# Performance work log

Measured on AMD Instinct MI355X. Metric: run time of the kernel, lower is better.

## Reference

```python
import jax, jax.numpy as jnp
import numpy as np

N_NODES, N_EDGES = 50000, 800000
IN_DIM, HID, HEADS, OUT_DIM = 256, 32, 8, 16
NEG_SLOPE = 0.2  # PyG GATConv default leaky-relu slope
EPS = 1e-16      # PyG softmax denominator epsilon


def setup_inputs() -> dict:
    key = jax.random.key(0)
    ks = jax.random.split(key, 12)
    x = jax.random.normal(ks[0], (N_NODES, IN_DIM), dtype=jnp.float32)
    edge_index = jax.random.randint(ks[1], (2, N_EDGES), 0, N_NODES, dtype=jnp.int32)
    s1 = 1.0 / np.sqrt(IN_DIM)
    s2 = 1.0 / np.sqrt(HID * HEADS)
    return {
        "x": x,
        "edge_index": edge_index,
        "W1": jax.random.normal(ks[2], (IN_DIM, HEADS * HID), dtype=jnp.float32) * s1,
        "att_src1": jax.random.normal(ks[3], (HEADS, HID), dtype=jnp.float32) * s1,
        "att_dst1": jax.random.normal(ks[4], (HEADS, HID), dtype=jnp.float32) * s1,
        "bias1": jnp.zeros((HEADS * HID,), dtype=jnp.float32),
        "W2": jax.random.normal(ks[5], (HEADS * HID, HEADS * OUT_DIM), dtype=jnp.float32) * s2,
        "att_src2": jax.random.normal(ks[6], (HEADS, OUT_DIM), dtype=jnp.float32) * s2,
        "att_dst2": jax.random.normal(ks[7], (HEADS, OUT_DIM), dtype=jnp.float32) * s2,
        "bias2": jnp.zeros((OUT_DIM,), dtype=jnp.float32),
    }


def _gat_conv(x, src, dst, W, att_src, att_dst, bias, concat):
    # x: [N, F_in]; src/dst: [E'] (self-loops already appended)
    N = x.shape[0]
    H, C = att_src.shape
    h = (x @ W).reshape(N, H, C)                      # [N, H, C]
    a_src = jnp.einsum('nhc,hc->nh', h, att_src)      # [N, H]
    a_dst = jnp.einsum('nhc,hc->nh', h, att_dst)
    e = a_src[src] + a_dst[dst]                       # [E', H]
    e = jax.nn.leaky_relu(e, NEG_SLOPE)
    # segment softmax over edges grouped by destination node
    m = jax.ops.segment_max(e, dst, num_segments=N)   # [N, H]
    e = jnp.exp(e - m[dst])
    denom = jax.ops.segment_sum(e, dst, num_segments=N)
    alpha = e / (denom[dst] + EPS)                    # [E', H]
    msg = h[src] * alpha[:, :, None]                  # [E', H, C] gather+weight
    out = jax.ops.segment_sum(msg, dst, num_segments=N)  # [N, H, C] scatter-add
    if concat:
        out = out.reshape(N, H * C)
    else:
        out = out.mean(axis=1)
    return out + bias


def reference(x, edge_index, W1, att_src1, att_dst1, bias1, W2, att_src2, att_dst2, bias2):
    N = x.shape[0]
    loop = jnp.arange(N, dtype=edge_index.dtype)
    src = jnp.concatenate([edge_index[0], loop])  # PyG add_self_loops=True
    dst = jnp.concatenate([edge_index[1], loop])
    h = _gat_conv(x, src, dst, W1, att_src1, att_dst1, bias1, concat=True)
    h = jax.nn.elu(h)
    out = _gat_conv(h, src, dst, W2, att_src2, att_dst2, bias2, concat=False)
    return out
```

## Files before the change

### kernel.cpp

```cpp
#include <hip/hip_runtime.h>

#define N_NODES 50000
#define N_EDGES 800000
#define EP (N_EDGES + N_NODES)
#define HEADS 8
#define NEG 0.2f

typedef __attribute__((ext_vector_type(8))) short bf16x8;
typedef __attribute__((ext_vector_type(8))) unsigned short u16x8;
typedef __attribute__((ext_vector_type(4))) float f32x4;

#define E_BLOCKS ((EP + 255) / 256)
#define MT_BLOCKS ((N_NODES + 63) / 64)
#define SCAN_BLOCKS 196
#define W_ITEMS  (65536 + 32768)
#define W_BLOCKS ((W_ITEMS + 255) / 256)


__device__ __forceinline__ float bf2f(unsigned short u) {
    return __uint_as_float(((unsigned)u) << 16);
}
__device__ __forceinline__ unsigned short f2bf(float f) {
    unsigned u = __float_as_uint(f);
    return (unsigned short)((u + 0x7FFFu + ((u >> 16) & 1u)) >> 16);
}

__device__ __forceinline__ void get_edge(const int* __restrict__ ei, int e, int& s, int& d) {
    if (e < N_EDGES) { s = ei[e]; d = ei[N_EDGES + e]; }
    else             { s = d = e - N_EDGES; }
}

__device__ __forceinline__ float lrelu(float v) { return v > 0.f ? v : NEG * v; }


__global__ void zero_wprep(int* __restrict__ cnt,
                           const float* __restrict__ W1, const float* __restrict__ W2,
                           unsigned short* __restrict__ W1T, unsigned short* __restrict__ W2T) {
    const int b = blockIdx.x;
    if (b < SCAN_BLOCKS) {
        int idx = b * 256 + threadIdx.x;
        if (idx < N_NODES) cnt[idx] = 0;
    } else {
        int t = (b - SCAN_BLOCKS) * 256 + threadIdx.x;
        if (t < 65536) {
            int k = t >> 8, n = t & 255;
            W1T[n * 256 + k] = f2bf(W1[k * 256 + n]);
        } else if (t < W_ITEMS) {
            int u = t - 65536; int k = u >> 7, n = u & 127;
            W2T[n * 256 + k] = f2bf(W2[k * 128 + n]);
        }
    }
}


__global__ void hist_kernel(const int* __restrict__ ei, int* __restrict__ cnt) {
    int e = blockIdx.x * 256 + threadIdx.x;
    if (e >= EP) return;
    int s, d; get_edge(ei, e, s, d);
    atomicAdd(&cnt[d], 1);
}


__global__ __launch_bounds__(256) void scan_p1(const int* __restrict__ cnt,
                                               int* __restrict__ incl, int* __restrict__ bsum) {
    __shared__ int wsum[4];
    const int tid = threadIdx.x, lane = tid & 63, wid = tid >> 6;
    const int idx = blockIdx.x * 256 + tid;
    int v = (idx < N_NODES) ? cnt[idx] : 0;
#pragma unroll
    for (int off = 1; off < 64; off <<= 1) {
        int t = __shfl_up(v, off);
        if (lane >= off) v += t;
    }
    if (lane == 63) wsum[wid] = v;
    __syncthreads();
    int add = 0;
#pragma unroll
    for (int w = 0; w < 4; w++) add += (w < wid) ? wsum[w] : 0;
    incl[idx] = v + add;
    if (tid == 255) bsum[blockIdx.x] = v + add;
}

__global__ __launch_bounds__(256) void scan_p23(const int* __restrict__ incl,
                                                const int* __restrict__ bsum,
                                                int* __restrict__ cnt_cursor,
                                                int* __restrict__ row_start) {
    __shared__ int sb[256];
    __shared__ int wsum[4];
    const int tid = threadIdx.x, lane = tid & 63, wid = tid >> 6;
    int v = (tid < SCAN_BLOCKS) ? bsum[tid] : 0;
#pragma unroll
    for (int off = 1; off < 64; off <<= 1) {
        int t = __shfl_up(v, off);
        if (lane >= off) v += t;
    }
    if (lane == 63) wsum[wid] = v;
    __syncthreads();
    int add = 0;
#pragma unroll
    for (int w = 0; w < 4; w++) add += (w < wid) ? wsum[w] : 0;
    sb[tid] = v + add;
    __syncthreads();
    const int bex = (blockIdx.x == 0) ? 0 : sb[blockIdx.x - 1];
    const int idx = blockIdx.x * 256 + tid;
    if (idx == 0) row_start[N_NODES] = EP;
    if (idx >= N_NODES) return;
    int ex = bex + incl[idx] - cnt_cursor[idx];
    row_start[idx] = ex;
    cnt_cursor[idx] = ex;
}


template<int NC, int C, bool AF32>
__device__ __forceinline__ void gemm_body(int bx, const void* __restrict__ Aptr,
        const unsigned short* __restrict__ WT,
        const float* __restrict__ att_s, const float* __restrict__ att_d,
        unsigned short* __restrict__ outh,
        float* __restrict__ a_src, float* __restrict__ a_dst) {
    constexpr int WN  = NC / 4;
    constexpr int NT  = WN / 16;
    constexpr int TPH = C / 16;
    constexpr int BJ  = NC / 32;
    __shared__ unsigned short As[64 * 64];
    __shared__ unsigned short Bs[NC * 64];
    const int m0 = bx * 64;
    const int tid  = threadIdx.x;
    const int wave = tid >> 6, lane = tid & 63;
    const int col = lane & 15, quad = lane >> 4;
    const int ar = tid >> 2;
    const int ac = tid & 3;
    const int arow = min(m0 + ar, N_NODES - 1);

    f32x4 acc[4][NT] = {};

    for (int k0 = 0; k0 < 256; k0 += 64) {
        u16x8 av[2];
        if constexpr (AF32) {
            const float* Af = (const float*)Aptr;
#pragma unroll
            for (int j = 0; j < 2; j++) {
                const float* p = Af + (size_t)arow * 256 + k0 + (ac + j * 4) * 8;
                float4 f0 = *(const float4*)p;
                float4 f1 = *(const float4*)(p + 4);
                u16x8 v;
                v[0] = f2bf(f0.x); v[1] = f2bf(f0.y); v[2] = f2bf(f0.z); v[3] = f2bf(f0.w);
                v[4] = f2bf(f1.x); v[5] = f2bf(f1.y); v[6] = f2bf(f1.z); v[7] = f2bf(f1.w);
                av[j] = v;
            }
        } else {
            const unsigned short* Ab = (const unsigned short*)Aptr;
#pragma unroll
            for (int j = 0; j < 2; j++)
                av[j] = *(const u16x8*)(Ab + (size_t)arow * 256 + k0 + (ac + j * 4) * 8);
        }
        u16x8 bv[BJ];
#pragma unroll
        for (int j = 0; j < BJ; j++) {
            int idx = j * 256 + tid, row = idx >> 3, ch = idx & 7;
            bv[j] = *(const u16x8*)(WT + (size_t)row * 256 + k0 + ch * 8);
        }
        __syncthreads();
#pragma unroll
        for (int j = 0; j < 2; j++) {
            int ch = ac + j * 4;
            *(u16x8*)&As[ar * 64 + (ch ^ (ar & 7)) * 8] = av[j];
        }
#pragma unroll
        for (int j = 0; j < BJ; j++) {
            int idx = j * 256 + tid, row = idx >> 3, ch = idx & 7;
            *(u16x8*)&Bs[row * 64 + (ch ^ (row & 7)) * 8] = bv[j];
        }
        __syncthreads();
#pragma unroll
        for (int ks = 0; ks < 64; ks += 32) {
            bf16x8 af[4], bfm[NT];
#pragma unroll
            for (int mi = 0; mi < 4; mi++) {
                int r = mi * 16 + col, c = (ks >> 3) + quad;
                af[mi] = *(const bf16x8*)&As[r * 64 + (c ^ (r & 7)) * 8];
            }
#pragma unroll
            for (int ni = 0; ni < NT; ni++) {
                int r = wave * WN + ni * 16 + col, c = (ks >> 3) + quad;
                bfm[ni] = *(const bf16x8*)&Bs[r * 64 + (c ^ (r & 7)) * 8];
            }
#pragma unroll
            for (int mi = 0; mi < 4; mi++)
#pragma unroll
                for (int ni = 0; ni < NT; ni++)
                    acc[mi][ni] = __builtin_amdgcn_mfma_f32_16x16x32_bf16(
                        af[mi], bfm[ni], acc[mi][ni], 0, 0, 0);
        }
    }

#pragma unroll
    for (int mi = 0; mi < 4; mi++)
#pragma unroll
        for (int ni = 0; ni < NT; ni++)
#pragma unroll
            for (int r = 0; r < 4; r++) {
                int m = m0 + mi * 16 + quad * 4 + r;
                if (m < N_NODES)
                    outh[(size_t)m * NC + wave * WN + ni * 16 + col] = f2bf(acc[mi][ni][r]);
            }

    float asv[NT], adv[NT];
#pragma unroll
    for (int ni = 0; ni < NT; ni++) {
        int n = wave * WN + ni * 16 + col;
        asv[ni] = att_s[n];
        adv[ni] = att_d[n];
    }
#pragma unroll
    for (int mi = 0; mi < 4; mi++)
#pragma unroll
        for (int r = 0; r < 4; r++) {
#pragma unroll
            for (int hl = 0; hl < 2; hl++) {
                float s = 0.f, d = 0.f;
#pragma unroll
                for (int t = 0; t < TPH; t++) {
                    int ni = hl * TPH + t;
                    s = fmaf(acc[mi][ni][r], asv[ni], s);
                    d = fmaf(acc[mi][ni][r], adv[ni], d);
                }
#pragma unroll
                for (int off = 1; off < 16; off <<= 1) {
                    s += __shfl_xor(s, off);
                    d += __shfl_xor(d, off);
                }
                if (col == 0) {
                    int m = m0 + mi * 16 + quad * 4 + r;
                    if (m < N_NODES) {
                        int hh = wave * 2 + hl;
                        a_src[m * 8 + hh] = s;
                        a_dst[m * 8 + hh] = d;
                    }
                }
            }
        }
}


__global__ __launch_bounds__(256) void gemm1_fill(const float* __restrict__ x,
        const unsigned short* __restrict__ W1T,
        const float* __restrict__ att_s, const float* __restrict__ att_d,
        unsigned short* __restrict__ outh,
        float* __restrict__ a_src, float* __restrict__ a_dst,
        const int* __restrict__ ei, int* __restrict__ cursor,
        unsigned short* __restrict__ csr) {
    if (blockIdx.x < MT_BLOCKS) {
        gemm_body<256, 32, true>(blockIdx.x, x, W1T, att_s, att_d, outh, a_src, a_dst);
    } else {
        int e = (blockIdx.x - MT_BLOCKS) * 256 + threadIdx.x;
        if (e >= EP) return;
        int s, d; get_edge(ei, e, s, d);
        int pos = atomicAdd(&cursor[d], 1);
        csr[pos] = (unsigned short)s;
    }
}

__global__ __launch_bounds__(256) void gemm2_kernel(const unsigned short* __restrict__ x2b,
        const unsigned short* __restrict__ W2T,
        const float* __restrict__ att_s, const float* __restrict__ att_d,
        unsigned short* __restrict__ outh,
        float* __restrict__ a_src, float* __restrict__ a_dst) {
    gemm_body<128, 16, false>(blockIdx.x, x2b, W2T, att_s, att_d, outh, a_src, a_dst);
}


__global__ __launch_bounds__(256) void gat_agg_l1(const int* __restrict__ row_start,
        const unsigned short* __restrict__ csr,
        const unsigned short* __restrict__ hfeat, const float* __restrict__ a_src,
        const float* __restrict__ a_dst, const float* __restrict__ bias,
        unsigned short* __restrict__ outp) {
    const int n    = blockIdx.x * 4 + (threadIdx.x >> 6);
    const int lane = threadIdx.x & 63;
    if (n >= N_NODES) return;

    const int rs  = row_start[n];
    const int deg = row_start[n + 1] - rs;
    const int p   = lane >> 5;
    const int q   = lane & 31;
    const int hq  = q >> 2;
    const float adstf = a_dst[n * 8 + hq];

    float acc[8] = {};
    float den = 0.f;

    for (int c0 = 0; c0 < deg; c0 += 64) {
        const int cnt = min(64, deg - c0);
        int myid = (lane < cnt) ? (int)csr[rs + c0 + lane] : 0;
        int e = 0;
        for (; e + 8 <= cnt; e += 8) {
            int ss[4];
#pragma unroll
            for (int j = 0; j < 4; j++) ss[j] = __shfl(myid, e + j * 2 + p);
            float as[4];
#pragma unroll
            for (int j = 0; j < 4; j++) as[j] = a_src[ss[j] * 8 + hq];
            u16x8 v[4];
#pragma unroll
            for (int j = 0; j < 4; j++)
                v[j] = *(const u16x8*)(hfeat + (size_t)ss[j] * 256 + q * 8);
#pragma unroll
            for (int j = 0; j < 4; j++) {
                float w = __expf(lrelu(as[j] + adstf));
                den += w;
#pragma unroll
                for (int k = 0; k < 8; k++)
                    acc[k] = fmaf(w, bf2f(v[j][k]), acc[k]);
            }
        }
        for (; e < cnt; e += 2) {
            int idx = e + p;
            bool ok = idx < cnt;
            int s = __shfl(myid, ok ? idx : cnt - 1);
            float w = ok ? __expf(lrelu(a_src[s * 8 + hq] + adstf)) : 0.f;
            den += w;
            u16x8 v = *(const u16x8*)(hfeat + (size_t)s * 256 + q * 8);
#pragma unroll
            for (int k = 0; k < 8; k++)
                acc[k] = fmaf(w, bf2f(v[k]), acc[k]);
        }
    }

    den += __shfl_xor(den, 32);
#pragma unroll
    for (int k = 0; k < 8; k++) acc[k] += __shfl_xor(acc[k], 32);

    if (p == 0) {
        const float inv = 1.f / (den + 1e-16f);
        float4 b0 = *(const float4*)(bias + q * 8);
        float4 b1 = *(const float4*)(bias + q * 8 + 4);
        float bb[8] = {b0.x, b0.y, b0.z, b0.w, b1.x, b1.y, b1.z, b1.w};
        u16x8 o;
#pragma unroll
        for (int k = 0; k < 8; k++) {
            float v = acc[k] * inv + bb[k];
            o[k] = f2bf(v > 0.f ? v : __expf(v) - 1.f);
        }
        *(u16x8*)(outp + (size_t)n * 256 + q * 8) = o;
    }
}


__global__ __launch_bounds__(256) void gat_agg_l2(const int* __restrict__ row_start,
        const unsigned short* __restrict__ csr,
        const unsigned short* __restrict__ hfeat, const float* __restrict__ a_src,
        const float* __restrict__ a_dst, const float* __restrict__ bias,
        float* __restrict__ outp) {
    const int n    = blockIdx.x * 4 + (threadIdx.x >> 6);
    const int lane = threadIdx.x & 63;
    if (n >= N_NODES) return;

    const int rs  = row_start[n];
    const int deg = row_start[n + 1] - rs;
    const int hf  = lane >> 3;
    const float adstf = a_dst[n * 8 + hf];

    float acc0 = 0.f, acc1 = 0.f, den = 0.f;

    for (int c0 = 0; c0 < deg; c0 += 64) {
        const int cnt = min(64, deg - c0);
        int myid = (lane < cnt) ? (int)csr[rs + c0 + lane] : 0;
        int e = 0;
        for (; e + 8 <= cnt; e += 8) {
            int ss[8];
#pragma unroll
            for (int j = 0; j < 8; j++) ss[j] = __shfl(myid, e + j);
            float as[8];
#pragma unroll
            for (int j = 0; j < 8; j++) as[j] = a_src[ss[j] * 8 + hf];
            ushort2 v[8];
#pragma unroll
            for (int j = 0; j < 8; j++)
                v[j] = *(const ushort2*)(hfeat + (size_t)ss[j] * 128 + lane * 2);
#pragma unroll
            for (int j = 0; j < 8; j++) {
                float w = __expf(lrelu(as[j] + adstf));
                den += w;
                acc0 = fmaf(w, bf2f(v[j].x), acc0);
                acc1 = fmaf(w, bf2f(v[j].y), acc1);
            }
        }
        for (; e < cnt; e++) {
            int s = __shfl(myid, e);
            float w = __expf(lrelu(a_src[s * 8 + hf] + adstf));
            den += w;
            ushort2 hv = *(const ushort2*)(hfeat + (size_t)s * 128 + lane * 2);
            acc0 = fmaf(w, bf2f(hv.x), acc0);
            acc1 = fmaf(w, bf2f(hv.y), acc1);
        }
    }

    const float inv = 1.f / (den + 1e-16f);
    float a0 = acc0 * inv, a1 = acc1 * inv;
#pragma unroll
    for (int off = 8; off <= 32; off <<= 1) {
        a0 += __shfl_xor(a0, off);
        a1 += __shfl_xor(a1, off);
    }
    if (lane < 8) {
        float2 o;
        o.x = a0 * 0.125f + bias[lane * 2 + 0];
        o.y = a1 * 0.125f + bias[lane * 2 + 1];
        *(float2*)(outp + (size_t)n * 16 + lane * 2) = o;
    }
}


extern "C" void kernel_launch(void* const* d_in, const int* in_sizes, int n_in,
                              void* d_out, int out_size, void* d_ws, size_t ws_size,
                              hipStream_t stream) {
    const float* x        = (const float*)d_in[0];
    const int*   ei       = (const int*)d_in[1];
    const float* W1       = (const float*)d_in[2];
    const float* att_src1 = (const float*)d_in[3];
    const float* att_dst1 = (const float*)d_in[4];
    const float* bias1    = (const float*)d_in[5];
    const float* W2       = (const float*)d_in[6];
    const float* att_src2 = (const float*)d_in[7];
    const float* att_dst2 = (const float*)d_in[8];
    const float* bias2    = (const float*)d_in[9];
    float* out = (float*)d_out;

    char* ws = (char*)d_ws;
    unsigned short* h1  = (unsigned short*)(ws);
    unsigned short* h2  = (unsigned short*)(ws);
    unsigned short* x2b = (unsigned short*)(ws + 32ull * 1024 * 1024);
    unsigned short* W1T = (unsigned short*)(ws + 64ull * 1024 * 1024);
    unsigned short* W2T = W1T + 65536;
    char* aux = ws + 66ull * 1024 * 1024;
    float*          a_src     = (float*)(aux);
    float*          a_dst     = (float*)(aux + 1600000);
    int*            row_start = (int*)  (aux + 3200000);
    int*            cnt       = (int*)  (aux + 3400064);
    unsigned short* csr       = (unsigned short*)(aux + 3600128);
    int*            incl      = (int*)  (aux + 5300128);
    int*            bsum      = (int*)  (aux + 5500832);

    const int AGG_BLOCKS = (N_NODES + 3) / 4;

    zero_wprep<<<SCAN_BLOCKS + W_BLOCKS, 256, 0, stream>>>(cnt, W1, W2, W1T, W2T);
    hist_kernel<<<E_BLOCKS, 256, 0, stream>>>(ei, cnt);
    scan_p1<<<SCAN_BLOCKS, 256, 0, stream>>>(cnt, incl, bsum);
    scan_p23<<<SCAN_BLOCKS, 256, 0, stream>>>(incl, bsum, cnt, row_start);

    gemm1_fill<<<MT_BLOCKS + E_BLOCKS, 256, 0, stream>>>(x, W1T, att_src1, att_dst1,
                                                         h1, a_src, a_dst, ei, cnt, csr);
    gat_agg_l1<<<AGG_BLOCKS, 256, 0, stream>>>(row_start, csr, h1, a_src, a_dst, bias1, x2b);

    gemm2_kernel<<<MT_BLOCKS, 256, 0, stream>>>(x2b, W2T, att_src2, att_dst2, h2, a_src, a_dst);
    gat_agg_l2<<<AGG_BLOCKS, 256, 0, stream>>>(row_start, csr, h2, a_src, a_dst, bias2, out);
}
```

Measured before the change: 333.5 us.

## Pre-convert x to bf16 and load GEMM fragments directly from global memory

```diff
diff --git a/kernel.cpp b/kernel.cpp
--- a/kernel.cpp
+++ b/kernel.cpp
@@ -13,6 +13,7 @@
 #define E_BLOCKS ((EP + 255) / 256)
 #define MT_BLOCKS ((N_NODES + 63) / 64)
 #define SCAN_BLOCKS 196
+#define X_BLOCKS 12500
 #define W_ITEMS  (65536 + 32768)
 #define W_BLOCKS ((W_ITEMS + 255) / 256)
 
@@ -33,15 +34,22 @@
 __device__ __forceinline__ float lrelu(float v) { return v > 0.f ? v : NEG * v; }
 
 
-__global__ void zero_wprep(int* __restrict__ cnt,
-                           const float* __restrict__ W1, const float* __restrict__ W2,
-                           unsigned short* __restrict__ W1T, unsigned short* __restrict__ W2T) {
+__global__ void prep_kernel(const float* __restrict__ x, int* __restrict__ cnt,
+                            const float* __restrict__ W1, const float* __restrict__ W2,
+                            unsigned short* __restrict__ xb,
+                            unsigned short* __restrict__ W1T, unsigned short* __restrict__ W2T) {
     const int b = blockIdx.x;
-    if (b < SCAN_BLOCKS) {
-        int idx = b * 256 + threadIdx.x;
+    if (b < X_BLOCKS) {
+        int t = b * 256 + threadIdx.x;
+        float4 v = ((const float4*)x)[t];
+        ushort4 o;
+        o.x = f2bf(v.x); o.y = f2bf(v.y); o.z = f2bf(v.z); o.w = f2bf(v.w);
+        ((ushort4*)xb)[t] = o;
+    } else if (b < X_BLOCKS + SCAN_BLOCKS) {
+        int idx = (b - X_BLOCKS) * 256 + threadIdx.x;
         if (idx < N_NODES) cnt[idx] = 0;
     } else {
-        int t = (b - SCAN_BLOCKS) * 256 + threadIdx.x;
+        int t = (b - X_BLOCKS - SCAN_BLOCKS) * 256 + threadIdx.x;
         if (t < 65536) {
             int k = t >> 8, n = t & 255;
             W1T[n * 256 + k] = f2bf(W1[k * 256 + n]);
@@ -111,8 +119,9 @@
 }
 
 
-template<int NC, int C, bool AF32>
-__device__ __forceinline__ void gemm_body(int bx, const void* __restrict__ Aptr,
+template<int NC, int C>
+__device__ __forceinline__ void gemm_body(int bx,
+        const unsigned short* __restrict__ A,
         const unsigned short* __restrict__ WT,
         const float* __restrict__ att_s, const float* __restrict__ att_d,
         unsigned short* __restrict__ outh,
@@ -120,76 +129,48 @@
     constexpr int WN  = NC / 4;
     constexpr int NT  = WN / 16;
     constexpr int TPH = C / 16;
-    constexpr int BJ  = NC / 32;
-    __shared__ unsigned short As[64 * 64];
-    __shared__ unsigned short Bs[NC * 64];
-    const int m0 = bx * 64;
     const int tid  = threadIdx.x;
     const int wave = tid >> 6, lane = tid & 63;
     const int col = lane & 15, quad = lane >> 4;
-    const int ar = tid >> 2;
-    const int ac = tid & 3;
-    const int arow = min(m0 + ar, N_NODES - 1);
+    const int m0 = bx * 64;
+
+    const unsigned short* ap[4];
+    const unsigned short* bp[NT];
+#pragma unroll
+    for (int mi = 0; mi < 4; mi++)
+        ap[mi] = A + (size_t)(m0 + mi * 16 + col) * 256 + quad * 8;
+#pragma unroll
+    for (int ni = 0; ni < NT; ni++)
+        bp[ni] = WT + (size_t)(wave * WN + ni * 16 + col) * 256 + quad * 8;
 
     f32x4 acc[4][NT] = {};
-
-    for (int k0 = 0; k0 < 256; k0 += 64) {
-        u16x8 av[2];
-        if constexpr (AF32) {
-            const float* Af = (const float*)Aptr;
-#pragma unroll
-            for (int j = 0; j < 2; j++) {
-                const float* p = Af + (size_t)arow * 256 + k0 + (ac + j * 4) * 8;
-                float4 f0 = *(const float4*)p;
-                float4 f1 = *(const float4*)(p + 4);
-                u16x8 v;
-                v[0] = f2bf(f0.x); v[1] = f2bf(f0.y); v[2] = f2bf(f0.z); v[3] = f2bf(f0.w);
-                v[4] = f2bf(f1.x); v[5] = f2bf(f1.y); v[6] = f2bf(f1.z); v[7] = f2bf(f1.w);
-                av[j] = v;
-            }
-        } else {
-            const unsigned short* Ab = (const unsigned short*)Aptr;
-#pragma unroll
-            for (int j = 0; j < 2; j++)
-                av[j] = *(const u16x8*)(Ab + (size_t)arow * 256 + k0 + (ac + j * 4) * 8);
-        }
-        u16x8 bv[BJ];
-#pragma unroll
-        for (int j = 0; j < BJ; j++) {
-            int idx = j * 256 + tid, row = idx >> 3, ch = idx & 7;
-            bv[j] = *(const u16x8*)(WT + (size_t)row * 256 + k0 + ch * 8);
-        }
-        __syncthreads();
-#pragma unroll
-        for (int j = 0; j < 2; j++) {
-            int ch = ac + j * 4;
-            *(u16x8*)&As[ar * 64 + (ch ^ (ar & 7)) * 8] = av[j];
-        }
-#pragma unroll
-        for (int j = 0; j < BJ; j++) {
-            int idx = j * 256 + tid, row = idx >> 3, ch = idx & 7;
-            *(u16x8*)&Bs[row * 64 + (ch ^ (row & 7)) * 8] = bv[j];
-        }
-        __syncthreads();
-#pragma unroll
-        for (int ks = 0; ks < 64; ks += 32) {
-            bf16x8 af[4], bfm[NT];
-#pragma unroll
-            for (int mi = 0; mi < 4; mi++) {
-                int r = mi * 16 + col, c = (ks >> 3) + quad;
-                af[mi] = *(const bf16x8*)&As[r * 64 + (c ^ (r & 7)) * 8];
-            }
-#pragma unroll
-            for (int ni = 0; ni < NT; ni++) {
-                int r = wave * WN + ni * 16 + col, c = (ks >> 3) + quad;
-                bfm[ni] = *(const bf16x8*)&Bs[r * 64 + (c ^ (r & 7)) * 8];
-            }
-#pragma unroll
-            for (int mi = 0; mi < 4; mi++)
-#pragma unroll
-                for (int ni = 0; ni < NT; ni++)
-                    acc[mi][ni] = __builtin_amdgcn_mfma_f32_16x16x32_bf16(
-                        af[mi], bfm[ni], acc[mi][ni], 0, 0, 0);
+    bf16x8 caf[4], cbf[NT];
+#pragma unroll
+    for (int mi = 0; mi < 4; mi++) caf[mi] = *(const bf16x8*)(ap[mi]);
+#pragma unroll
+    for (int ni = 0; ni < NT; ni++) cbf[ni] = *(const bf16x8*)(bp[ni]);
+
+#pragma unroll
+    for (int s = 0; s < 8; s++) {
+        bf16x8 naf[4], nbf[NT];
+        if (s < 7) {
+            const int k1 = (s + 1) * 32;
+#pragma unroll
+            for (int mi = 0; mi < 4; mi++) naf[mi] = *(const bf16x8*)(ap[mi] + k1);
+#pragma unroll
+            for (int ni = 0; ni < NT; ni++) nbf[ni] = *(const bf16x8*)(bp[ni] + k1);
+        }
+#pragma unroll
+        for (int mi = 0; mi < 4; mi++)
+#pragma unroll
+            for (int ni = 0; ni < NT; ni++)
+                acc[mi][ni] = __builtin_amdgcn_mfma_f32_16x16x32_bf16(
+                    caf[mi], cbf[ni], acc[mi][ni], 0, 0, 0);
+        if (s < 7) {
+#pragma unroll
+            for (int mi = 0; mi < 4; mi++) caf[mi] = naf[mi];
+#pragma unroll
+            for (int ni = 0; ni < NT; ni++) cbf[ni] = nbf[ni];
         }
     }
 
@@ -242,7 +223,7 @@
 }
 
 
-__global__ __launch_bounds__(256) void gemm1_fill(const float* __restrict__ x,
+__global__ __launch_bounds__(256) void gemm1_fill(const unsigned short* __restrict__ xb,
         const unsigned short* __restrict__ W1T,
         const float* __restrict__ att_s, const float* __restrict__ att_d,
         unsigned short* __restrict__ outh,
@@ -250,7 +231,7 @@
         const int* __restrict__ ei, int* __restrict__ cursor,
         unsigned short* __restrict__ csr) {
     if (blockIdx.x < MT_BLOCKS) {
-        gemm_body<256, 32, true>(blockIdx.x, x, W1T, att_s, att_d, outh, a_src, a_dst);
+        gemm_body<256, 32>(blockIdx.x, xb, W1T, att_s, att_d, outh, a_src, a_dst);
     } else {
         int e = (blockIdx.x - MT_BLOCKS) * 256 + threadIdx.x;
         if (e >= EP) return;
@@ -265,7 +246,7 @@
         const float* __restrict__ att_s, const float* __restrict__ att_d,
         unsigned short* __restrict__ outh,
         float* __restrict__ a_src, float* __restrict__ a_dst) {
-    gemm_body<128, 16, false>(blockIdx.x, x2b, W2T, att_s, att_d, outh, a_src, a_dst);
+    gemm_body<128, 16>(blockIdx.x, x2b, W2T, att_s, att_d, outh, a_src, a_dst);
 }
 
 
@@ -431,7 +412,8 @@
     unsigned short* x2b = (unsigned short*)(ws + 32ull * 1024 * 1024);
     unsigned short* W1T = (unsigned short*)(ws + 64ull * 1024 * 1024);
     unsigned short* W2T = W1T + 65536;
-    char* aux = ws + 66ull * 1024 * 1024;
+    unsigned short* xb  = (unsigned short*)(ws + 66ull * 1024 * 1024);
+    char* aux = ws + 96ull * 1024 * 1024;
     float*          a_src     = (float*)(aux);
     float*          a_dst     = (float*)(aux + 1600000);
     int*            row_start = (int*)  (aux + 3200000);
@@ -442,12 +424,12 @@
 
     const int AGG_BLOCKS = (N_NODES + 3) / 4;
 
-    zero_wprep<<<SCAN_BLOCKS + W_BLOCKS, 256, 0, stream>>>(cnt, W1, W2, W1T, W2T);
+    prep_kernel<<<X_BLOCKS + SCAN_BLOCKS + W_BLOCKS, 256, 0, stream>>>(x, cnt, W1, W2, xb, W1T, W2T);
     hist_kernel<<<E_BLOCKS, 256, 0, stream>>>(ei, cnt);
     scan_p1<<<SCAN_BLOCKS, 256, 0, stream>>>(cnt, incl, bsum);
     scan_p23<<<SCAN_BLOCKS, 256, 0, stream>>>(incl, bsum, cnt, row_start);
 
-    gemm1_fill<<<MT_BLOCKS + E_BLOCKS, 256, 0, stream>>>(x, W1T, att_src1, att_dst1,
+    gemm1_fill<<<MT_BLOCKS + E_BLOCKS, 256, 0, stream>>>(xb, W1T, att_src1, att_dst1,
                                                          h1, a_src, a_dst, ei, cnt, csr);
     gat_agg_l1<<<AGG_BLOCKS, 256, 0, stream>>>(row_start, csr, h1, a_src, a_dst, bias1, x2b);
 
```

Result: slower. 360.4 us (+8.0%).
